# Kernel tuning notes

Measured on AMD Instinct MI355X. Metric: run time of the kernel, lower is better.

The kernel has to match this reference:

```python
import jax, jax.numpy as jnp
import numpy as np

B, M, N = 8, 8192, 8192  # batch, input neurons, output neurons
SPIKE_CAP = 0.9          # VPRTempo caps spike amplitude at 0.9


def setup_inputs() -> dict:
    key = jax.random.key(0)
    k0, k1, k2, k3 = jax.random.split(key, 4)
    # pre-synaptic spike amplitudes in [0, 1)
    pre_spikes = jax.random.uniform(k0, (B, 1, M), dtype=jnp.float32)
    # combined excitatory+inhibitory weights
    W = jax.random.normal(k1, (M, N), dtype=jnp.float32) * 0.01
    # per-neuron thresholds, uniform in thr_range = [0, 0.5]
    thr = jax.random.uniform(k2, (B, 1, N), dtype=jnp.float32) * 0.5
    # per-neuron constant input, uniform in const_inp = [0, 0.1]
    const_inp = jax.random.uniform(k3, (B, 1, N), dtype=jnp.float32) * 0.1
    return {"pre_spikes": pre_spikes, "W": W, "thr": thr, "const_inp": const_inp}


def reference(pre_spikes, W, thr, const_inp):
    # membrane potential: weighted pre-synaptic spikes + constant input
    x = jnp.einsum('bom,mn->bon', pre_spikes, W) + const_inp  # [B,1,N]
    # spike generation: amplitude above threshold, clamped to [0, 0.9]
    spikes = jnp.clip(x - thr, 0.0, SPIKE_CAP)
    return spikes
```

## Files before the change

kernel.cpp:

```cpp
#include <hip/hip_runtime.h>


constexpr int Mdim = 8192;
constexpr int Ndim = 8192;
constexpr int Bdim = 8;
constexpr int PANELS  = 4;
constexpr int PANEL_N = Ndim / PANELS;
constexpr int CHUNKS  = 128;
constexpr int CROWS   = Mdim / CHUNKS;
constexpr float CAP = 0.9f;

__global__ __launch_bounds__(256, 2) void snn_stage1(
    const float* __restrict__ pre,
    const float* __restrict__ W,
    float* __restrict__ part)
{
    __shared__ float lds_pre[Bdim * CROWS];

    const int t     = threadIdx.x;
    const int panel = blockIdx.x;
    const int chunk = blockIdx.y;
    const int r0    = chunk * CROWS;
    const int colA  = panel * PANEL_N + t * 4;
    const int colB  = colA + 1024;

    for (int q = t; q < Bdim * CROWS; q += 256) {
        int b = q >> 6, j = q & 63;
        lds_pre[q] = pre[b * Mdim + r0 + j];
    }
    __syncthreads();

    float4 accA[Bdim], accB[Bdim];
#pragma unroll
    for (int b = 0; b < Bdim; ++b) {
        accA[b] = make_float4(0.f, 0.f, 0.f, 0.f);
        accB[b] = make_float4(0.f, 0.f, 0.f, 0.f);
    }

    const int phase = (blockIdx.y * 5 + blockIdx.x) & 15;
    for (int i = 0; i < 16; ++i) {
        const int rr = ((i + phase) & 15) * 4;
        const int r  = r0 + rr;

        float4 wA[4], wB[4];
#pragma unroll
        for (int j = 0; j < 4; ++j) {
            const float* row = W + (size_t)(r + j) * Ndim;
            wA[j] = *reinterpret_cast<const float4*>(row + colA);
            wB[j] = *reinterpret_cast<const float4*>(row + colB);
        }

        float4 pf[Bdim];
#pragma unroll
        for (int b = 0; b < Bdim; ++b)
            pf[b] = *reinterpret_cast<const float4*>(lds_pre + b * CROWS + rr);

#pragma unroll
        for (int b = 0; b < Bdim; ++b) {
            float4 a = accA[b], c = accB[b];
            a.x = fmaf(pf[b].x, wA[0].x, a.x); a.y = fmaf(pf[b].x, wA[0].y, a.y);
            a.z = fmaf(pf[b].x, wA[0].z, a.z); a.w = fmaf(pf[b].x, wA[0].w, a.w);
            c.x = fmaf(pf[b].x, wB[0].x, c.x); c.y = fmaf(pf[b].x, wB[0].y, c.y);
            c.z = fmaf(pf[b].x, wB[0].z, c.z); c.w = fmaf(pf[b].x, wB[0].w, c.w);

            a.x = fmaf(pf[b].y, wA[1].x, a.x); a.y = fmaf(pf[b].y, wA[1].y, a.y);
            a.z = fmaf(pf[b].y, wA[1].z, a.z); a.w = fmaf(pf[b].y, wA[1].w, a.w);
            c.x = fmaf(pf[b].y, wB[1].x, c.x); c.y = fmaf(pf[b].y, wB[1].y, c.y);
            c.z = fmaf(pf[b].y, wB[1].z, c.z); c.w = fmaf(pf[b].y, wB[1].w, c.w);

            a.x = fmaf(pf[b].z, wA[2].x, a.x); a.y = fmaf(pf[b].z, wA[2].y, a.y);
            a.z = fmaf(pf[b].z, wA[2].z, a.z); a.w = fmaf(pf[b].z, wA[2].w, a.w);
            c.x = fmaf(pf[b].z, wB[2].x, c.x); c.y = fmaf(pf[b].z, wB[2].y, c.y);
            c.z = fmaf(pf[b].z, wB[2].z, c.z); c.w = fmaf(pf[b].z, wB[2].w, c.w);

            a.x = fmaf(pf[b].w, wA[3].x, a.x); a.y = fmaf(pf[b].w, wA[3].y, a.y);
            a.z = fmaf(pf[b].w, wA[3].z, a.z); a.w = fmaf(pf[b].w, wA[3].w, a.w);
            c.x = fmaf(pf[b].w, wB[3].x, c.x); c.y = fmaf(pf[b].w, wB[3].y, c.y);
            c.z = fmaf(pf[b].w, wB[3].z, c.z); c.w = fmaf(pf[b].w, wB[3].w, c.w);
            accA[b] = a; accB[b] = c;
        }
    }

    float* ps = part + (size_t)chunk * (Bdim * Ndim);
#pragma unroll
    for (int b = 0; b < Bdim; ++b) {
        *reinterpret_cast<float4*>(ps + (size_t)b * Ndim + colA) = accA[b];
        *reinterpret_cast<float4*>(ps + (size_t)b * Ndim + colB) = accB[b];
    }
}

__global__ __launch_bounds__(256, 4) void snn_stage2(
    const float* __restrict__ part,
    const float* __restrict__ thr,
    const float* __restrict__ cst,
    float* __restrict__ out)
{
    const int bid = blockIdx.x;
    const int i = bid * 256 + threadIdx.x;
    float s = 0.f;
#pragma unroll 8
    for (int k = 0; k < CHUNKS; ++k) {
        int kk = (k + bid) & (CHUNKS - 1);
        s += part[(size_t)kk * (Bdim * Ndim) + i];
    }
    float x = s + cst[i] - thr[i];
    x = fminf(fmaxf(x, 0.f), CAP);
    out[i] = x;
}

extern "C" void kernel_launch(void* const* d_in, const int* in_sizes, int n_in,
                              void* d_out, int out_size, void* d_ws, size_t ws_size,
                              hipStream_t stream) {
    const float* pre = (const float*)d_in[0];
    const float* W   = (const float*)d_in[1];
    const float* thr = (const float*)d_in[2];
    const float* cst = (const float*)d_in[3];
    float* out  = (float*)d_out;
    float* part = (float*)d_ws;

    dim3 g1(PANELS, CHUNKS);
    hipLaunchKernelGGL(snn_stage1, g1, dim3(256), 0, stream, pre, W, part);

    dim3 g2((Bdim * Ndim) / 256);
    hipLaunchKernelGGL(snn_stage2, g2, dim3(256), 0, stream, part, thr, cst, out);
}
```

Measured before the change: 368.1 us.

## Halve split-K chunks, widen panels, and double-buffer weight loads

```diff
diff --git a/kernel.cpp b/kernel.cpp
--- a/kernel.cpp
+++ b/kernel.cpp
@@ -4,9 +4,9 @@
 constexpr int Mdim = 8192;
 constexpr int Ndim = 8192;
 constexpr int Bdim = 8;
-constexpr int PANELS  = 4;
+constexpr int PANELS  = 8;
 constexpr int PANEL_N = Ndim / PANELS;
-constexpr int CHUNKS  = 128;
+constexpr int CHUNKS  = 64;
 constexpr int CROWS   = Mdim / CHUNKS;
 constexpr float CAP = 0.9f;
 
@@ -21,72 +21,68 @@
     const int panel = blockIdx.x;
     const int chunk = blockIdx.y;
     const int r0    = chunk * CROWS;
-    const int colA  = panel * PANEL_N + t * 4;
-    const int colB  = colA + 1024;
+    const int col   = panel * PANEL_N + t * 4;
 
+#pragma unroll
     for (int q = t; q < Bdim * CROWS; q += 256) {
-        int b = q >> 6, j = q & 63;
+        int b = q >> 7, j = q & 127;
         lds_pre[q] = pre[b * Mdim + r0 + j];
     }
+
+    float4 acc[Bdim];
+#pragma unroll
+    for (int b = 0; b < Bdim; ++b) acc[b] = make_float4(0.f, 0.f, 0.f, 0.f);
+
+    const float* wcol = W + col;
+    const int phase = (chunk * 5 + panel * 11) & 15;
+    auto rowoff = [&](int i) { return ((i + phase) & 15) * 8; };
+
+    auto loadW = [&](float4* w, int rr) {
+        const float* base = wcol + (size_t)(r0 + rr) * Ndim;
+#pragma unroll
+        for (int j = 0; j < 8; ++j)
+            w[j] = *reinterpret_cast<const float4*>(base + (size_t)j * Ndim);
+    };
+
+    auto compute = [&](const float4* w, int rr) {
+#pragma unroll
+        for (int half = 0; half < 2; ++half) {
+            const float4 w0 = w[4 * half], w1 = w[4 * half + 1],
+                         w2 = w[4 * half + 2], w3 = w[4 * half + 3];
+#pragma unroll
+            for (int b = 0; b < Bdim; ++b) {
+                float4 p = *reinterpret_cast<const float4*>(
+                    lds_pre + b * CROWS + rr + 4 * half);
+                float4 a = acc[b];
+                a.x = fmaf(p.x, w0.x, a.x); a.y = fmaf(p.x, w0.y, a.y);
+                a.z = fmaf(p.x, w0.z, a.z); a.w = fmaf(p.x, w0.w, a.w);
+                a.x = fmaf(p.y, w1.x, a.x); a.y = fmaf(p.y, w1.y, a.y);
+                a.z = fmaf(p.y, w1.z, a.z); a.w = fmaf(p.y, w1.w, a.w);
+                a.x = fmaf(p.z, w2.x, a.x); a.y = fmaf(p.z, w2.y, a.y);
+                a.z = fmaf(p.z, w2.z, a.z); a.w = fmaf(p.z, w2.w, a.w);
+                a.x = fmaf(p.w, w3.x, a.x); a.y = fmaf(p.w, w3.y, a.y);
+                a.z = fmaf(p.w, w3.z, a.z); a.w = fmaf(p.w, w3.w, a.w);
+                acc[b] = a;
+            }
+        }
+    };
+
+    float4 wa[8], wb[8];
+    loadW(wa, rowoff(0));
     __syncthreads();
 
-    float4 accA[Bdim], accB[Bdim];
 #pragma unroll
-    for (int b = 0; b < Bdim; ++b) {
-        accA[b] = make_float4(0.f, 0.f, 0.f, 0.f);
-        accB[b] = make_float4(0.f, 0.f, 0.f, 0.f);
-    }
-
-    const int phase = (blockIdx.y * 5 + blockIdx.x) & 15;
-    for (int i = 0; i < 16; ++i) {
-        const int rr = ((i + phase) & 15) * 4;
-        const int r  = r0 + rr;
-
-        float4 wA[4], wB[4];
-#pragma unroll
-        for (int j = 0; j < 4; ++j) {
-            const float* row = W + (size_t)(r + j) * Ndim;
-            wA[j] = *reinterpret_cast<const float4*>(row + colA);
-            wB[j] = *reinterpret_cast<const float4*>(row + colB);
-        }
-
-        float4 pf[Bdim];
-#pragma unroll
-        for (int b = 0; b < Bdim; ++b)
-            pf[b] = *reinterpret_cast<const float4*>(lds_pre + b * CROWS + rr);
-
-#pragma unroll
-        for (int b = 0; b < Bdim; ++b) {
-            float4 a = accA[b], c = accB[b];
-            a.x = fmaf(pf[b].x, wA[0].x, a.x); a.y = fmaf(pf[b].x, wA[0].y, a.y);
-            a.z = fmaf(pf[b].x, wA[0].z, a.z); a.w = fmaf(pf[b].x, wA[0].w, a.w);
-            c.x = fmaf(pf[b].x, wB[0].x, c.x); c.y = fmaf(pf[b].x, wB[0].y, c.y);
-            c.z = fmaf(pf[b].x, wB[0].z, c.z); c.w = fmaf(pf[b].x, wB[0].w, c.w);
-
-            a.x = fmaf(pf[b].y, wA[1].x, a.x); a.y = fmaf(pf[b].y, wA[1].y, a.y);
-            a.z = fmaf(pf[b].y, wA[1].z, a.z); a.w = fmaf(pf[b].y, wA[1].w, a.w);
-            c.x = fmaf(pf[b].y, wB[1].x, c.x); c.y = fmaf(pf[b].y, wB[1].y, c.y);
-            c.z = fmaf(pf[b].y, wB[1].z, c.z); c.w = fmaf(pf[b].y, wB[1].w, c.w);
-
-            a.x = fmaf(pf[b].z, wA[2].x, a.x); a.y = fmaf(pf[b].z, wA[2].y, a.y);
-            a.z = fmaf(pf[b].z, wA[2].z, a.z); a.w = fmaf(pf[b].z, wA[2].w, a.w);
-            c.x = fmaf(pf[b].z, wB[2].x, c.x); c.y = fmaf(pf[b].z, wB[2].y, c.y);
-            c.z = fmaf(pf[b].z, wB[2].z, c.z); c.w = fmaf(pf[b].z, wB[2].w, c.w);
-
-            a.x = fmaf(pf[b].w, wA[3].x, a.x); a.y = fmaf(pf[b].w, wA[3].y, a.y);
-            a.z = fmaf(pf[b].w, wA[3].z, a.z); a.w = fmaf(pf[b].w, wA[3].w, a.w);
-            c.x = fmaf(pf[b].w, wB[3].x, c.x); c.y = fmaf(pf[b].w, wB[3].y, c.y);
-            c.z = fmaf(pf[b].w, wB[3].z, c.z); c.w = fmaf(pf[b].w, wB[3].w, c.w);
-            accA[b] = a; accB[b] = c;
-        }
+    for (int ii = 0; ii < 8; ++ii) {
+        loadW(wb, rowoff(2 * ii + 1));
+        compute(wa, rowoff(2 * ii));
+        if (ii < 7) loadW(wa, rowoff(2 * ii + 2));
+        compute(wb, rowoff(2 * ii + 1));
     }
 
     float* ps = part + (size_t)chunk * (Bdim * Ndim);
 #pragma unroll
-    for (int b = 0; b < Bdim; ++b) {
-        *reinterpret_cast<float4*>(ps + (size_t)b * Ndim + colA) = accA[b];
-        *reinterpret_cast<float4*>(ps + (size_t)b * Ndim + colB) = accB[b];
-    }
+    for (int b = 0; b < Bdim; ++b)
+        *reinterpret_cast<float4*>(ps + (size_t)b * Ndim + col) = acc[b];
 }
 
 __global__ __launch_bounds__(256, 4) void snn_stage2(
@@ -100,7 +96,7 @@
     float s = 0.f;
 #pragma unroll 8
     for (int k = 0; k < CHUNKS; ++k) {
-        int kk = (k + bid) & (CHUNKS - 1);
+        int kk = (k + bid * 7) & (CHUNKS - 1);
         s += part[(size_t)kk * (Bdim * Ndim) + i];
     }
     float x = s + cst[i] - thr[i];
```

Measured after the change: 362.0 us. About the same (-1.7%).
